# Performance work log

Measured on AMD Instinct MI355X. Metric: run time of the kernel, lower is better.

The kernel has to match this reference:

```python
import jax, jax.numpy as jnp
import numpy as np


def setup_inputs() -> dict:
    key = jax.random.key(0)
    ks = jax.random.split(key, 16)
    B, S, D, H = 32, 2048, 512, 512
    s = 1.0 / np.sqrt(H)
    inp = {
        "x": jax.random.normal(ks[0], (B, H), jnp.float32),
        "context": jax.random.normal(ks[1], (B, S, D), jnp.float32),
        "mask": jnp.zeros((B, S), jnp.bool_),  # False = valid position
        "Wi": jax.random.normal(ks[2], (H, H), jnp.float32) * s,
        "bi": jax.random.normal(ks[3], (H,), jnp.float32) * s,
        "Wc0": jax.random.normal(ks[4], (H, D), jnp.float32) * s,
        "bc0": jax.random.normal(ks[5], (H,), jnp.float32) * s,
        "Wc1": jax.random.normal(ks[6], (H, D), jnp.float32) * s,
        "bc1": jax.random.normal(ks[7], (H,), jnp.float32) * s,
        "Wc2": jax.random.normal(ks[8], (H, D), jnp.float32) * s,
        "bc2": jax.random.normal(ks[9], (H,), jnp.float32) * s,
        "Wc3": jax.random.normal(ks[10], (H, D), jnp.float32) * s,
        "bc3": jax.random.normal(ks[11], (H,), jnp.float32) * s,
        "V": jax.random.uniform(ks[12], (H,), jnp.float32, -s, s),
    }
    return inp


def reference(x, context, mask, Wi, bi, Wc0, bc0, Wc1, bc1, Wc2, bc2, Wc3, bc3, V):
    # mask: True = masked out in the original API; module flips it first.
    valid = ~mask  # [B, S], True = keep

    inp = (x @ Wi.T + bi)[:, :, None]  # [B, H, 1]

    def proj(W, b):
        # Conv1d(D, H, kernel=1) on context.permute(0,2,1) == token-wise GEMM
        return jnp.einsum("bsd,hd->bhs", context, W) + b[None, :, None]  # [B, H, S]

    ctx = jnp.concatenate(
        [proj(Wc0, bc0), proj(Wc1, bc1), proj(Wc2, bc2), proj(Wc3, bc3)], axis=2
    )  # [B, H, 4S]

    t = jnp.tanh(inp + ctx)                      # [B, H, 4S]
    att = jnp.einsum("h,bhs->bs", V, t)          # bmm(V[B,1,H], t).squeeze(1)
    att = 10.0 * jnp.tanh(att)                   # [B, 4S]

    valid4 = jnp.tile(valid, (1, 4))             # mask.repeat(1, 4)
    att = jnp.where(valid4, att, -jnp.inf)
    # torch.no_grad() around the masked fill detaches the rest of the graph
    att = jax.lax.stop_gradient(att)

    ans = jax.nn.softmax(att, axis=1)            # [B, 4S]
    p = jnp.max(ans, axis=1)
    indices = jnp.argmax(ans, axis=1)
    return indices[:, None], p[:, None], mask
```

## Files before the change

kernel.cpp:

```cpp
#include <hip/hip_runtime.h>
#include <math.h>

typedef __bf16 bf16x8 __attribute__((ext_vector_type(8)));
typedef float f32x4 __attribute__((ext_vector_type(4)));
typedef short short8v __attribute__((ext_vector_type(8)));

#define MARGIN 0.01f
#define NCAND 32

#define WAITL  do { asm volatile("s_waitcnt lgkmcnt(0)" ::: "memory"); __builtin_amdgcn_sched_barrier(0); } while (0)
#define WAITV0 do { asm volatile("s_waitcnt vmcnt(0)" ::: "memory"); __builtin_amdgcn_sched_barrier(0); } while (0)
#define WAITV4 do { asm volatile("s_waitcnt vmcnt(4)" ::: "memory"); __builtin_amdgcn_sched_barrier(0); } while (0)
#define WAITV8 do { asm volatile("s_waitcnt vmcnt(8)" ::: "memory"); __builtin_amdgcn_sched_barrier(0); } while (0)
#define BARR   do { __builtin_amdgcn_s_barrier(); __builtin_amdgcn_sched_barrier(0); } while (0)

__device__ __forceinline__ unsigned short f2bf(float f) {
  unsigned u = __float_as_uint(f);
  u += 0x7fffu + ((u >> 16) & 1u);
  return (unsigned short)(u >> 16);
}
__device__ __forceinline__ float tanh_fast(float x) {
  float e = __builtin_amdgcn_exp2f(x * 2.885390081777927f);
  return 1.f - 2.f * __builtin_amdgcn_rcpf(e + 1.f);
}
__device__ __forceinline__ void gl_lds16(const void* g, void* l) {
  __builtin_amdgcn_global_load_lds(
      (const __attribute__((address_space(1))) unsigned int*)g,
      (__attribute__((address_space(3))) unsigned int*)l, 16, 0, 0);
}
__device__ __forceinline__ float dpp_row_reduce(float v) {
  int x;
  x = __builtin_amdgcn_update_dpp(0, __builtin_bit_cast(int, v), 0x118, 0xf, 0xf, true);
  v += __builtin_bit_cast(float, x);
  x = __builtin_amdgcn_update_dpp(0, __builtin_bit_cast(int, v), 0x114, 0xf, 0xf, true);
  v += __builtin_bit_cast(float, x);
  x = __builtin_amdgcn_update_dpp(0, __builtin_bit_cast(int, v), 0x112, 0xf, 0xf, true);
  v += __builtin_bit_cast(float, x);
  x = __builtin_amdgcn_update_dpp(0, __builtin_bit_cast(int, v), 0x111, 0xf, 0xf, true);
  v += __builtin_bit_cast(float, x);
  return v;
}

__global__ __launch_bounds__(256) void prep_inp_k(const float* __restrict__ x,
    const float* __restrict__ Wi, const float* __restrict__ bi, float* __restrict__ inp) {
  int gid = blockIdx.x * 256 + threadIdx.x;
  int b = gid >> 9, h = gid & 511;
  const float* xr = x + b * 512;
  const float* wr = Wi + h * 512;
  float acc = bi[h];
  #pragma unroll 4
  for (int k = 0; k < 512; k += 4) {
    float4 xv = *(const float4*)(xr + k);
    float4 wv = *(const float4*)(wr + k);
    acc += xv.x * wv.x + xv.y * wv.y + xv.z * wv.z + xv.w * wv.w;
  }
  inp[gid] = acc;
}

__global__ __launch_bounds__(256) void prep_w_pack_k(const float* __restrict__ w0,
    const float* __restrict__ w1, const float* __restrict__ w2, const float* __restrict__ w3,
    short* __restrict__ Whi) {
  int gid = blockIdx.x * 256 + threadIdx.x;
  if (gid >= 131072) return;
  int c = gid & 3, row = (gid >> 2) & 255, TK = gid >> 10;
  int TN = TK >> 4, KS = TK & 15;
  int n = TN * 256 + row;
  int g = n >> 9, h = n & 511;
  const float* w = (g == 0) ? w0 : (g == 1) ? w1 : (g == 2) ? w2 : w3;
  const float* src = w + (size_t)h * 512 + KS * 32 + c * 8;
  float f[8];
  *(float4*)&f[0] = *(const float4*)(src);
  *(float4*)&f[4] = *(const float4*)(src + 4);
  short8v hv;
  #pragma unroll
  for (int i = 0; i < 8; ++i) hv[i] = (short)f2bf(f[i]);
  *(short8v*)(Whi + (size_t)gid * 8) = hv;
}

__global__ __launch_bounds__(256) void prep_ctx_pack_k(const float* __restrict__ ctx,
    short* __restrict__ Chi) {
  int gid = blockIdx.x * 256 + threadIdx.x;
  int c = gid & 3, row = (gid >> 2) & 255, TK = gid >> 10;
  int TM = TK >> 4, KS = TK & 15;
  size_t m = (size_t)TM * 256 + row;
  int k = KS * 32 + c * 8;
  float f[8];
  *(float4*)&f[0] = *(const float4*)(ctx + m * 512 + k);
  *(float4*)&f[4] = *(const float4*)(ctx + m * 512 + k + 4);
  short8v hv;
  #pragma unroll
  for (int i = 0; i < 8; ++i) hv[i] = (short)f2bf(f[i]);
  *(short8v*)(Chi + (size_t)gid * 8) = hv;
}

template<bool PRESPLIT>
__global__ __launch_bounds__(512, 2) void gemm_att_k(
    const float* __restrict__ ctx, const short* __restrict__ Chi,
    const short* __restrict__ Whi,
    const float* __restrict__ inp,
    const float* __restrict__ bc0, const float* __restrict__ bc1,
    const float* __restrict__ bc2, const float* __restrict__ bc3,
    const float* __restrict__ V, float* __restrict__ att) {
  __shared__ __align__(16) short smem[4][2][8192];
  __shared__ float sV[256], sPre[256];

  const int t = threadIdx.x;
  int d = blockIdx.x + (blockIdx.y << 3);
  int work = (d & 7) * 256 + (d >> 3);
  int mt = work >> 3, nt = work & 7;
  int b = mt >> 3;
  int g = nt >> 1, h0 = (nt & 1) * 256;

  if (t < 256) {
    const float* bc = (g == 0) ? bc0 : (g == 1) ? bc1 : (g == 2) ? bc2 : bc3;
    sV[t] = V[h0 + t];
    sPre[t] = inp[b * 512 + h0 + t] + bc[h0 + t];
  }

  const int toff = t * 8;
  auto stageA = [&](int tile) {
    const short* gA = Chi + (((size_t)mt * 16 + tile) << 13) + toff;
    short* lA = &smem[tile & 3][0][0];
    gl_lds16(gA,        lA + toff);
    gl_lds16(gA + 4096, lA + toff + 4096);
  };
  auto stageB = [&](int tile) {
    const short* gB = Whi + (((size_t)nt * 16 + tile) << 13) + toff;
    short* lB = &smem[tile & 3][1][0];
    gl_lds16(gB,        lB + toff);
    gl_lds16(gB + 4096, lB + toff + 4096);
  };
  auto stageA_reg = [&](int tile) {
    #pragma unroll
    for (int pass = 0; pass < 2; ++pass) {
      int cc = pass * 512 + t;
      int c = cc & 3, r = cc >> 2;
      int k = tile * 32 + c * 8;
      const float* src = ctx + ((size_t)mt * 256 + r) * 512 + k;
      float f[8];
      *(float4*)&f[0] = *(const float4*)src;
      *(float4*)&f[4] = *(const float4*)(src + 4);
      short8v hv;
      #pragma unroll
      for (int i = 0; i < 8; ++i) hv[i] = (short)f2bf(f[i]);
      *(short8v*)(&smem[tile & 3][0][r * 32 + c * 8]) = hv;
    }
  };

  f32x4 acc[8][4];
  #pragma unroll
  for (int i = 0; i < 8; ++i)
    #pragma unroll
    for (int j = 0; j < 4; ++j) acc[i][j] = (f32x4){0.f, 0.f, 0.f, 0.f};

  const int lane = t & 63, wid = t >> 6;
  const int wr = wid >> 2, wc = wid & 3;
  const int fr = lane & 15, fq = lane >> 4;
  const int abase = (wr * 128 + fr) * 32 + fq * 8;
  const int bbase = (wc * 64 + fr) * 32 + fq * 8;

  if constexpr (PRESPLIT) {
    stageA(0); stageB(0); stageA(1); stageB(1); stageA(2); stageB(2);
    WAITV8;
  } else {
    stageA_reg(0); stageB(0);
    WAITV0; WAITL;
  }
  BARR;

  #pragma unroll 4
  for (int tt = 0; tt < 16; ++tt) {
    const short* sa = &smem[tt & 3][0][0];
    const short* sb = &smem[tt & 3][1][0];
    bf16x8 a[8], b0, b1, b2, b3;
    #pragma unroll
    for (int mi = 0; mi < 8; ++mi)
      a[mi] = *(const bf16x8*)(sa + abase + mi * 512);
    b0 = *(const bf16x8*)(sb + bbase);
    b1 = *(const bf16x8*)(sb + bbase + 512);
    b2 = *(const bf16x8*)(sb + bbase + 1024);
    b3 = *(const bf16x8*)(sb + bbase + 1536);
    WAITL;
    __builtin_amdgcn_s_setprio(1);
    #pragma unroll
    for (int mi = 0; mi < 8; ++mi) {
      acc[mi][0] = __builtin_amdgcn_mfma_f32_16x16x32_bf16(a[mi], b0, acc[mi][0], 0, 0, 0);
      acc[mi][1] = __builtin_amdgcn_mfma_f32_16x16x32_bf16(a[mi], b1, acc[mi][1], 0, 0, 0);
    }
    #pragma unroll
    for (int mi = 0; mi < 8; ++mi) {
      acc[mi][2] = __builtin_amdgcn_mfma_f32_16x16x32_bf16(a[mi], b2, acc[mi][2], 0, 0, 0);
      acc[mi][3] = __builtin_amdgcn_mfma_f32_16x16x32_bf16(a[mi], b3, acc[mi][3], 0, 0, 0);
    }
    __builtin_amdgcn_s_setprio(0);
    __builtin_amdgcn_sched_barrier(0);
    if constexpr (PRESPLIT) {
      if (tt <= 12) { stageA(tt + 3); stageB(tt + 3); }
      if (tt <= 12)      { WAITV8; }
      else if (tt == 13) { WAITV4; }
      else if (tt == 14) { WAITV0; }
    } else {
      if (tt < 15) { stageA_reg(tt + 1); stageB(tt + 1); WAITV0; WAITL; }
    }
    BARR;
  }

  float vV[4], vP[4];
  #pragma unroll
  for (int ni = 0; ni < 4; ++ni) {
    int j = wc * 64 + ni * 16 + fr;
    vV[ni] = sV[j];
    vP[ni] = sPre[j];
  }
  size_t abatt = (size_t)b * 8192 + (size_t)g * 2048;
  #pragma unroll
  for (int mi = 0; mi < 8; ++mi) {
    #pragma unroll
    for (int r = 0; r < 4; ++r) {
      float sum = 0.f;
      #pragma unroll
      for (int ni = 0; ni < 4; ++ni)
        sum += vV[ni] * tanh_fast(vP[ni] + acc[mi][ni][r]);
      sum = dpp_row_reduce(sum);
      if (fr == 15) {
        int s = (mt * 256 + wr * 128 + mi * 16 + fq * 4 + r) & 2047;
        atomicAdd(&att[abatt + s], sum);
      }
    }
  }
}

__global__ __launch_bounds__(256) void tail_k(const float* __restrict__ att,
    const unsigned char* __restrict__ mask, const float* __restrict__ ctx,
    const float* __restrict__ Wc0, const float* __restrict__ Wc1,
    const float* __restrict__ Wc2, const float* __restrict__ Wc3,
    const float* __restrict__ bc0, const float* __restrict__ bc1,
    const float* __restrict__ bc2, const float* __restrict__ bc3,
    const float* __restrict__ inp, const float* __restrict__ V,
    float* __restrict__ out) {
  int b = blockIdx.x, t = threadIdx.x;
  __shared__ float sred[256];
  __shared__ float sctx[512];
  __shared__ int scnt;
  __shared__ int scand_j[NCAND];
  __shared__ float scand_a[NCAND];
  __shared__ float sexact[NCAND];

  if (t == 0) scnt = 0;
  float bm = -1e30f;
  for (int j = t; j < 8192; j += 256) {
    if (mask[b * 2048 + (j & 2047)]) continue;
    bm = fmaxf(bm, att[(size_t)b * 8192 + j]);
  }
  sred[t] = bm;
  __syncthreads();
  for (int s2 = 128; s2 > 0; s2 >>= 1) {
    if (t < s2) sred[t] = fmaxf(sred[t], sred[t + s2]);
    __syncthreads();
  }
  float mx = sred[0];
  float Lref = 10.f * tanhf(mx);
  __syncthreads();
  float se = 0.f;
  for (int j = t; j < 8192; j += 256) {
    if (mask[b * 2048 + (j & 2047)]) continue;
    float a = att[(size_t)b * 8192 + j];
    se += expf(10.f * tanhf(a) - Lref);
    if (a >= mx - MARGIN) {
      int slot = atomicAdd(&scnt, 1);
      if (slot < NCAND) { scand_j[slot] = j; scand_a[slot] = a; }
    }
  }
  sred[t] = se;
  __syncthreads();
  for (int s2 = 128; s2 > 0; s2 >>= 1) {
    if (t < s2) sred[t] += sred[t + s2];
    __syncthreads();
  }
  float den = sred[0];
  int n = min(scnt, NCAND);
  for (int j = t; j < 2048; j += 256)
    out[64 + b * 2048 + j] = mask[b * 2048 + j] ? 1.0f : 0.0f;
  for (int i = 0; i < n; ++i) {
    int jj = scand_j[i];
    int g = jj >> 11, s = jj & 2047;
    const float* W  = (g == 0) ? Wc0 : (g == 1) ? Wc1 : (g == 2) ? Wc2 : Wc3;
    const float* bc = (g == 0) ? bc0 : (g == 1) ? bc1 : (g == 2) ? bc2 : bc3;
    const float* cr = ctx + ((size_t)b * 2048 + s) * 512;
    __syncthreads();
    sctx[t] = cr[t];
    sctx[t + 256] = cr[t + 256];
    __syncthreads();
    float total = 0.f;
    #pragma unroll
    for (int hh = 0; hh < 2; ++hh) {
      int h = t + hh * 256;
      const float* wrp = W + (size_t)h * 512;
      float acc = 0.f;
      #pragma unroll 4
      for (int k = 0; k < 512; k += 4) {
        float4 wv = *(const float4*)(wrp + k);
        acc += wv.x * sctx[k] + wv.y * sctx[k + 1] + wv.z * sctx[k + 2] + wv.w * sctx[k + 3];
      }
      total += V[h] * tanhf(inp[b * 512 + h] + bc[h] + acc);
    }
    sred[t] = total;
    __syncthreads();
    for (int s2 = 128; s2 > 0; s2 >>= 1) {
      if (t < s2) sred[t] += sred[t + s2];
      __syncthreads();
    }
    if (t == 0) sexact[i] = sred[0];
  }
  __syncthreads();
  if (t == 0) {
    float dd = den, best = -1e30f;
    int bj = 0x7fffffff;
    for (int i = 0; i < n; ++i) {
      float e = sexact[i];
      int j = scand_j[i];
      dd += expf(10.f * tanhf(e) - Lref) - expf(10.f * tanhf(scand_a[i]) - Lref);
      if (e > best || (e == best && j < bj)) { best = e; bj = j; }
    }
    out[b] = (float)bj;
    out[32 + b] = expf(10.f * tanhf(best) - Lref) / dd;
  }
}

extern "C" void kernel_launch(void* const* d_in, const int* in_sizes, int n_in,
                              void* d_out, int out_size, void* d_ws, size_t ws_size,
                              hipStream_t stream) {
  const float* x    = (const float*)d_in[0];
  const float* ctx  = (const float*)d_in[1];
  const unsigned char* mask = (const unsigned char*)d_in[2];
  const float* Wi   = (const float*)d_in[3];
  const float* bi   = (const float*)d_in[4];
  const float* Wc0  = (const float*)d_in[5];
  const float* bc0  = (const float*)d_in[6];
  const float* Wc1  = (const float*)d_in[7];
  const float* bc1  = (const float*)d_in[8];
  const float* Wc2  = (const float*)d_in[9];
  const float* bc2  = (const float*)d_in[10];
  const float* Wc3  = (const float*)d_in[11];
  const float* bc3  = (const float*)d_in[12];
  const float* V    = (const float*)d_in[13];
  float* out = (float*)d_out;

  float* inp    = (float*)d_ws;
  float* att    = inp + 16384;
  short* Whi    = (short*)(att + 262144);
  short* Chi    = Whi + 1048576;
  size_t need = (size_t)((char*)(Chi + 33554432) - (char*)d_ws);
  bool presplit = ws_size >= need;

  hipMemsetAsync(att, 0, 262144 * sizeof(float), stream);
  prep_inp_k<<<64, 256, 0, stream>>>(x, Wi, bi, inp);
  prep_w_pack_k<<<512, 256, 0, stream>>>(Wc0, Wc1, Wc2, Wc3, Whi);
  if (presplit) {
    prep_ctx_pack_k<<<16384, 256, 0, stream>>>(ctx, Chi);
    gemm_att_k<true><<<dim3(8, 256), 512, 0, stream>>>(ctx, Chi, Whi,
        inp, bc0, bc1, bc2, bc3, V, att);
  } else {
    gemm_att_k<false><<<dim3(8, 256), 512, 0, stream>>>(ctx, nullptr, Whi,
        inp, bc0, bc1, bc2, bc3, V, att);
  }
  tail_k<<<32, 256, 0, stream>>>(att, mask, ctx, Wc0, Wc1, Wc2, Wc3,
      bc0, bc1, bc2, bc3, inp, V, out);
}
```

Baseline: 314.6 us.

## Load GEMM fragments directly from global into registers, dropping LDS staging

The presplit GEMM path no longer stages packed bf16 tiles through shared memory with a 4-deep async ring. Each wave now loads its MFMA fragments straight from the pre-packed global arrays into registers, double-buffered across K tiles with vmcnt-based waits. This removes LDS traffic and block barriers from the main loop. In exchange, data that several waves share is fetched redundantly from global/L2, and register pressure rises from holding two fragment sets. The fallback path is reduced to 2-stage LDS buffering.

After: 377.7 us. +20.0%, slower.

```diff
diff --git a/kernel.cpp b/kernel.cpp
--- a/kernel.cpp
+++ b/kernel.cpp
@@ -8,11 +8,10 @@
 #define MARGIN 0.01f
 #define NCAND 32
 
-#define WAITL  do { asm volatile("s_waitcnt lgkmcnt(0)" ::: "memory"); __builtin_amdgcn_sched_barrier(0); } while (0)
-#define WAITV0 do { asm volatile("s_waitcnt vmcnt(0)" ::: "memory"); __builtin_amdgcn_sched_barrier(0); } while (0)
-#define WAITV4 do { asm volatile("s_waitcnt vmcnt(4)" ::: "memory"); __builtin_amdgcn_sched_barrier(0); } while (0)
-#define WAITV8 do { asm volatile("s_waitcnt vmcnt(8)" ::: "memory"); __builtin_amdgcn_sched_barrier(0); } while (0)
-#define BARR   do { __builtin_amdgcn_s_barrier(); __builtin_amdgcn_sched_barrier(0); } while (0)
+#define WAITL   do { asm volatile("s_waitcnt lgkmcnt(0)" ::: "memory"); __builtin_amdgcn_sched_barrier(0); } while (0)
+#define WAITV0  do { asm volatile("s_waitcnt vmcnt(0)" ::: "memory"); __builtin_amdgcn_sched_barrier(0); } while (0)
+#define WAITV12 do { asm volatile("s_waitcnt vmcnt(12)" ::: "memory"); __builtin_amdgcn_sched_barrier(0); } while (0)
+#define BARR    do { __builtin_amdgcn_s_barrier(); __builtin_amdgcn_sched_barrier(0); } while (0)
 
 __device__ __forceinline__ unsigned short f2bf(float f) {
   unsigned u = __float_as_uint(f);
@@ -93,15 +92,34 @@
   *(short8v*)(Chi + (size_t)gid * 8) = hv;
 }
 
-template<bool PRESPLIT>
-__global__ __launch_bounds__(512, 2) void gemm_att_k(
-    const float* __restrict__ ctx, const short* __restrict__ Chi,
-    const short* __restrict__ Whi,
+#define LOADF(A_, B_, TT) do { \
+    const short* pa = Chi + aRegBase + (size_t)(TT) * 8192 + aoff; \
+    const short* pb = Whi + bRegBase + (size_t)(TT) * 8192 + boff; \
+    _Pragma("unroll") \
+    for (int mi = 0; mi < 8; ++mi) A_[mi] = *(const bf16x8*)(pa + mi * 512); \
+    _Pragma("unroll") \
+    for (int ni = 0; ni < 4; ++ni) B_[ni] = *(const bf16x8*)(pb + ni * 512); \
+  } while (0)
+
+#define MFMA_SET(A_, B_) do { \
+    __builtin_amdgcn_s_setprio(1); \
+    _Pragma("unroll") \
+    for (int mi = 0; mi < 8; ++mi) { \
+      acc[mi][0] = __builtin_amdgcn_mfma_f32_16x16x32_bf16(A_[mi], B_[0], acc[mi][0], 0, 0, 0); \
+      acc[mi][1] = __builtin_amdgcn_mfma_f32_16x16x32_bf16(A_[mi], B_[1], acc[mi][1], 0, 0, 0); \
+      acc[mi][2] = __builtin_amdgcn_mfma_f32_16x16x32_bf16(A_[mi], B_[2], acc[mi][2], 0, 0, 0); \
+      acc[mi][3] = __builtin_amdgcn_mfma_f32_16x16x32_bf16(A_[mi], B_[3], acc[mi][3], 0, 0, 0); \
+    } \
+    __builtin_amdgcn_s_setprio(0); \
+    __builtin_amdgcn_sched_barrier(0); \
+  } while (0)
+
+__global__ __launch_bounds__(512, 2) void gemm_direct_k(
+    const short* __restrict__ Chi, const short* __restrict__ Whi,
     const float* __restrict__ inp,
     const float* __restrict__ bc0, const float* __restrict__ bc1,
     const float* __restrict__ bc2, const float* __restrict__ bc3,
     const float* __restrict__ V, float* __restrict__ att) {
-  __shared__ __align__(16) short smem[4][2][8192];
   __shared__ float sV[256], sPre[256];
 
   const int t = threadIdx.x;
@@ -116,20 +134,83 @@
     sV[t] = V[h0 + t];
     sPre[t] = inp[b * 512 + h0 + t] + bc[h0 + t];
   }
-
+  __syncthreads();
+
+  const int lane = t & 63, wid = t >> 6;
+  const int wr = wid >> 2, wc = wid & 3;
+  const int fr = lane & 15, fq = lane >> 4;
+  const size_t aRegBase = (size_t)(mt * 16) * 8192;
+  const size_t bRegBase = (size_t)(nt * 16) * 8192;
+  const int aoff = (wr * 128 + fr) * 32 + fq * 8;
+  const int boff = (wc * 64 + fr) * 32 + fq * 8;
+
+  f32x4 acc[8][4];
+  #pragma unroll
+  for (int i = 0; i < 8; ++i)
+    #pragma unroll
+    for (int j = 0; j < 4; ++j) acc[i][j] = (f32x4){0.f, 0.f, 0.f, 0.f};
+
+  bf16x8 a0[8], b0v[4], a1[8], b1v[4];
+  LOADF(a0, b0v, 0);
+  #pragma unroll
+  for (int it = 0; it < 8; ++it) {
+    LOADF(a1, b1v, 2 * it + 1);
+    WAITV12;
+    MFMA_SET(a0, b0v);
+    if (it < 7) {
+      LOADF(a0, b0v, 2 * it + 2);
+      WAITV12;
+    } else {
+      WAITV0;
+    }
+    MFMA_SET(a1, b1v);
+  }
+
+  float vV[4], vP[4];
+  #pragma unroll
+  for (int ni = 0; ni < 4; ++ni) {
+    int j = wc * 64 + ni * 16 + fr;
+    vV[ni] = sV[j];
+    vP[ni] = sPre[j];
+  }
+  size_t abatt = (size_t)b * 8192 + (size_t)g * 2048;
+  #pragma unroll
+  for (int mi = 0; mi < 8; ++mi) {
+    #pragma unroll
+    for (int r = 0; r < 4; ++r) {
+      float sum = 0.f;
+      #pragma unroll
+      for (int ni = 0; ni < 4; ++ni)
+        sum += vV[ni] * tanh_fast(vP[ni] + acc[mi][ni][r]);
+      sum = dpp_row_reduce(sum);
+      if (fr == 15) {
+        int s = (mt * 256 + wr * 128 + mi * 16 + fq * 4 + r) & 2047;
+        atomicAdd(&att[abatt + s], sum);
+      }
+    }
+  }
+}
+
+__global__ __launch_bounds__(512, 2) void gemm_fallback_k(
+    const float* __restrict__ ctx, const short* __restrict__ Whi,
+    const float* __restrict__ inp,
+    const float* __restrict__ bc0, const float* __restrict__ bc1,
+    const float* __restrict__ bc2, const float* __restrict__ bc3,
+    const float* __restrict__ V, float* __restrict__ att) {
+  __shared__ __align__(16) short smem[2][2][8192];
+  __shared__ float sV[256], sPre[256];
+  const int t = threadIdx.x;
+  int d = blockIdx.x + (blockIdx.y << 3);
+  int work = (d & 7) * 256 + (d >> 3);
+  int mt = work >> 3, nt = work & 7;
+  int b = mt >> 3;
+  int g = nt >> 1, h0 = (nt & 1) * 256;
+  if (t < 256) {
+    const float* bc = (g == 0) ? bc0 : (g == 1) ? bc1 : (g == 2) ? bc2 : bc3;
+    sV[t] = V[h0 + t];
+    sPre[t] = inp[b * 512 + h0 + t] + bc[h0 + t];
+  }
   const int toff = t * 8;
-  auto stageA = [&](int tile) {
-    const short* gA = Chi + (((size_t)mt * 16 + tile) << 13) + toff;
-    short* lA = &smem[tile & 3][0][0];
-    gl_lds16(gA,        lA + toff);
-    gl_lds16(gA + 4096, lA + toff + 4096);
-  };
-  auto stageB = [&](int tile) {
-    const short* gB = Whi + (((size_t)nt * 16 + tile) << 13) + toff;
-    short* lB = &smem[tile & 3][1][0];
-    gl_lds16(gB,        lB + toff);
-    gl_lds16(gB + 4096, lB + toff + 4096);
-  };
   auto stageA_reg = [&](int tile) {
     #pragma unroll
     for (int pass = 0; pass < 2; ++pass) {
@@ -143,68 +224,44 @@
       short8v hv;
       #pragma unroll
       for (int i = 0; i < 8; ++i) hv[i] = (short)f2bf(f[i]);
-      *(short8v*)(&smem[tile & 3][0][r * 32 + c * 8]) = hv;
+      *(short8v*)(&smem[tile & 1][0][r * 32 + c * 8]) = hv;
     }
   };
-
+  auto stageB = [&](int tile) {
+    const short* gB = Whi + (((size_t)nt * 16 + tile) << 13) + toff;
+    short* lB = &smem[tile & 1][1][0];
+    gl_lds16(gB,        lB + toff);
+    gl_lds16(gB + 4096, lB + toff + 4096);
+  };
   f32x4 acc[8][4];
   #pragma unroll
   for (int i = 0; i < 8; ++i)
     #pragma unroll
     for (int j = 0; j < 4; ++j) acc[i][j] = (f32x4){0.f, 0.f, 0.f, 0.f};
-
   const int lane = t & 63, wid = t >> 6;
   const int wr = wid >> 2, wc = wid & 3;
   const int fr = lane & 15, fq = lane >> 4;
   const int abase = (wr * 128 + fr) * 32 + fq * 8;
   const int bbase = (wc * 64 + fr) * 32 + fq * 8;
-
-  if constexpr (PRESPLIT) {
-    stageA(0); stageB(0); stageA(1); stageB(1); stageA(2); stageB(2);
-    WAITV8;
-  } else {
-    stageA_reg(0); stageB(0);
-    WAITV0; WAITL;
-  }
+  stageA_reg(0); stageB(0);
+  WAITV0; WAITL;
   BARR;
-
-  #pragma unroll 4
   for (int tt = 0; tt < 16; ++tt) {
-    const short* sa = &smem[tt & 3][0][0];
-    const short* sb = &smem[tt & 3][1][0];
-    bf16x8 a[8], b0, b1, b2, b3;
+    const short* sa = &smem[tt & 1][0][0];
+    const short* sb = &smem[tt & 1][1][0];
+    bf16x8 a[8], bfr[4];
     #pragma unroll
     for (int mi = 0; mi < 8; ++mi)
       a[mi] = *(const bf16x8*)(sa + abase + mi * 512);
-    b0 = *(const bf16x8*)(sb + bbase);
-    b1 = *(const bf16x8*)(sb + bbase + 512);
-    b2 = *(const bf16x8*)(sb + bbase + 1024);
-    b3 = *(const bf16x8*)(sb + bbase + 1536);
+    bfr[0] = *(const bf16x8*)(sb + bbase);
+    bfr[1] = *(const bf16x8*)(sb + bbase + 512);
+    bfr[2] = *(const bf16x8*)(sb + bbase + 1024);
+    bfr[3] = *(const bf16x8*)(sb + bbase + 1536);
     WAITL;
-    __builtin_amdgcn_s_setprio(1);
-    #pragma unroll
-    for (int mi = 0; mi < 8; ++mi) {
-      acc[mi][0] = __builtin_amdgcn_mfma_f32_16x16x32_bf16(a[mi], b0, acc[mi][0], 0, 0, 0);
-      acc[mi][1] = __builtin_amdgcn_mfma_f32_16x16x32_bf16(a[mi], b1, acc[mi][1], 0, 0, 0);
-    }
-    #pragma unroll
-    for (int mi = 0; mi < 8; ++mi) {
-      acc[mi][2] = __builtin_amdgcn_mfma_f32_16x16x32_bf16(a[mi], b2, acc[mi][2], 0, 0, 0);
-      acc[mi][3] = __builtin_amdgcn_mfma_f32_16x16x32_bf16(a[mi], b3, acc[mi][3], 0, 0, 0);
-    }
-    __builtin_amdgcn_s_setprio(0);
-    __builtin_amdgcn_sched_barrier(0);
-    if constexpr (PRESPLIT) {
-      if (tt <= 12) { stageA(tt + 3); stageB(tt + 3); }
-      if (tt <= 12)      { WAITV8; }
-      else if (tt == 13) { WAITV4; }
-      else if (tt == 14) { WAITV0; }
-    } else {
-      if (tt < 15) { stageA_reg(tt + 1); stageB(tt + 1); WAITV0; WAITL; }
-    }
+    MFMA_SET(a, bfr);
+    if (tt < 15) { stageA_reg(tt + 1); stageB(tt + 1); WAITV0; WAITL; }
     BARR;
   }
-
   float vV[4], vP[4];
   #pragma unroll
   for (int ni = 0; ni < 4; ++ni) {
@@ -358,10 +415,10 @@
   prep_w_pack_k<<<512, 256, 0, stream>>>(Wc0, Wc1, Wc2, Wc3, Whi);
   if (presplit) {
     prep_ctx_pack_k<<<16384, 256, 0, stream>>>(ctx, Chi);
-    gemm_att_k<true><<<dim3(8, 256), 512, 0, stream>>>(ctx, Chi, Whi,
+    gemm_direct_k<<<dim3(8, 256), 512, 0, stream>>>(Chi, Whi,
         inp, bc0, bc1, bc2, bc3, V, att);
   } else {
-    gemm_att_k<false><<<dim3(8, 256), 512, 0, stream>>>(ctx, nullptr, Whi,
+    gemm_fallback_k<<<dim3(8, 256), 512, 0, stream>>>(ctx, Whi,
         inp, bc0, bc1, bc2, bc3, V, att);
   }
   tail_k<<<32, 256, 0, stream>>>(att, mask, ctx, Wc0, Wc1, Wc2, Wc3,
```

## Drop context pre-pack pass, convert context inside GEMM, merge prep kernels

Applied to the files above, without the earlier changes.

Removes the separate pass that converted the full context tensor to packed bf16 in workspace. The GEMM now always loads fp32 context through registers and converts it per tile, giving up the 3-deep async LDS pipeline for single-tile staging. The two small prep kernels are merged into one launch, and the tail kernel is widened to 1024 threads. The aim is to avoid writing and re-reading a large bf16 copy of context, at the cost of less load/compute overlap in the GEMM.

Result: slower. 339.5 us (+7.9%).

```diff
diff --git a/kernel.cpp b/kernel.cpp
--- a/kernel.cpp
+++ b/kernel.cpp
@@ -10,8 +10,6 @@
 
 #define WAITL  do { asm volatile("s_waitcnt lgkmcnt(0)" ::: "memory"); __builtin_amdgcn_sched_barrier(0); } while (0)
 #define WAITV0 do { asm volatile("s_waitcnt vmcnt(0)" ::: "memory"); __builtin_amdgcn_sched_barrier(0); } while (0)
-#define WAITV4 do { asm volatile("s_waitcnt vmcnt(4)" ::: "memory"); __builtin_amdgcn_sched_barrier(0); } while (0)
-#define WAITV8 do { asm volatile("s_waitcnt vmcnt(8)" ::: "memory"); __builtin_amdgcn_sched_barrier(0); } while (0)
 #define BARR   do { __builtin_amdgcn_s_barrier(); __builtin_amdgcn_sched_barrier(0); } while (0)
 
 __device__ __forceinline__ unsigned short f2bf(float f) {
@@ -41,62 +39,46 @@
   return v;
 }
 
-__global__ __launch_bounds__(256) void prep_inp_k(const float* __restrict__ x,
-    const float* __restrict__ Wi, const float* __restrict__ bi, float* __restrict__ inp) {
-  int gid = blockIdx.x * 256 + threadIdx.x;
-  int b = gid >> 9, h = gid & 511;
-  const float* xr = x + b * 512;
-  const float* wr = Wi + h * 512;
-  float acc = bi[h];
-  #pragma unroll 4
-  for (int k = 0; k < 512; k += 4) {
-    float4 xv = *(const float4*)(xr + k);
-    float4 wv = *(const float4*)(wr + k);
-    acc += xv.x * wv.x + xv.y * wv.y + xv.z * wv.z + xv.w * wv.w;
-  }
-  inp[gid] = acc;
-}
-
-__global__ __launch_bounds__(256) void prep_w_pack_k(const float* __restrict__ w0,
-    const float* __restrict__ w1, const float* __restrict__ w2, const float* __restrict__ w3,
-    short* __restrict__ Whi) {
-  int gid = blockIdx.x * 256 + threadIdx.x;
-  if (gid >= 131072) return;
-  int c = gid & 3, row = (gid >> 2) & 255, TK = gid >> 10;
-  int TN = TK >> 4, KS = TK & 15;
-  int n = TN * 256 + row;
-  int g = n >> 9, h = n & 511;
-  const float* w = (g == 0) ? w0 : (g == 1) ? w1 : (g == 2) ? w2 : w3;
-  const float* src = w + (size_t)h * 512 + KS * 32 + c * 8;
-  float f[8];
-  *(float4*)&f[0] = *(const float4*)(src);
-  *(float4*)&f[4] = *(const float4*)(src + 4);
-  short8v hv;
-  #pragma unroll
-  for (int i = 0; i < 8; ++i) hv[i] = (short)f2bf(f[i]);
-  *(short8v*)(Whi + (size_t)gid * 8) = hv;
-}
-
-__global__ __launch_bounds__(256) void prep_ctx_pack_k(const float* __restrict__ ctx,
-    short* __restrict__ Chi) {
-  int gid = blockIdx.x * 256 + threadIdx.x;
-  int c = gid & 3, row = (gid >> 2) & 255, TK = gid >> 10;
-  int TM = TK >> 4, KS = TK & 15;
-  size_t m = (size_t)TM * 256 + row;
-  int k = KS * 32 + c * 8;
-  float f[8];
-  *(float4*)&f[0] = *(const float4*)(ctx + m * 512 + k);
-  *(float4*)&f[4] = *(const float4*)(ctx + m * 512 + k + 4);
-  short8v hv;
-  #pragma unroll
-  for (int i = 0; i < 8; ++i) hv[i] = (short)f2bf(f[i]);
-  *(short8v*)(Chi + (size_t)gid * 8) = hv;
-}
-
-template<bool PRESPLIT>
-__global__ __launch_bounds__(512, 2) void gemm_att_k(
-    const float* __restrict__ ctx, const short* __restrict__ Chi,
-    const short* __restrict__ Whi,
+__global__ __launch_bounds__(256) void prep_small_k(
+    const float* __restrict__ x, const float* __restrict__ Wi,
+    const float* __restrict__ bi,
+    const float* __restrict__ w0, const float* __restrict__ w1,
+    const float* __restrict__ w2, const float* __restrict__ w3,
+    short* __restrict__ Whi, float* __restrict__ inp) {
+  int bid = blockIdx.x;
+  if (bid < 512) {
+    int gid = bid * 256 + threadIdx.x;
+    int c = gid & 3, row = (gid >> 2) & 255, TK = gid >> 10;
+    int TN = TK >> 4, KS = TK & 15;
+    int n = TN * 256 + row;
+    int g = n >> 9, h = n & 511;
+    const float* w = (g == 0) ? w0 : (g == 1) ? w1 : (g == 2) ? w2 : w3;
+    const float* src = w + (size_t)h * 512 + KS * 32 + c * 8;
+    float f[8];
+    *(float4*)&f[0] = *(const float4*)(src);
+    *(float4*)&f[4] = *(const float4*)(src + 4);
+    short8v hv;
+    #pragma unroll
+    for (int i = 0; i < 8; ++i) hv[i] = (short)f2bf(f[i]);
+    *(short8v*)(Whi + (size_t)gid * 8) = hv;
+  } else {
+    int gid = (bid - 512) * 256 + threadIdx.x;
+    int b = gid >> 9, h = gid & 511;
+    const float* xr = x + b * 512;
+    const float* wr = Wi + h * 512;
+    float acc = bi[h];
+    #pragma unroll 4
+    for (int k = 0; k < 512; k += 4) {
+      float4 xv = *(const float4*)(xr + k);
+      float4 wv = *(const float4*)(wr + k);
+      acc += xv.x * wv.x + xv.y * wv.y + xv.z * wv.z + xv.w * wv.w;
+    }
+    inp[gid] = acc;
+  }
+}
+
+__global__ __launch_bounds__(512, 2) void gemm_fused_k(
+    const float* __restrict__ ctx, const short* __restrict__ Whi,
     const float* __restrict__ inp,
     const float* __restrict__ bc0, const float* __restrict__ bc1,
     const float* __restrict__ bc2, const float* __restrict__ bc3,
@@ -119,18 +101,6 @@
 
   const int toff = t * 8;
   auto stageA = [&](int tile) {
-    const short* gA = Chi + (((size_t)mt * 16 + tile) << 13) + toff;
-    short* lA = &smem[tile & 3][0][0];
-    gl_lds16(gA,        lA + toff);
-    gl_lds16(gA + 4096, lA + toff + 4096);
-  };
-  auto stageB = [&](int tile) {
-    const short* gB = Whi + (((size_t)nt * 16 + tile) << 13) + toff;
-    short* lB = &smem[tile & 3][1][0];
-    gl_lds16(gB,        lB + toff);
-    gl_lds16(gB + 4096, lB + toff + 4096);
-  };
-  auto stageA_reg = [&](int tile) {
     #pragma unroll
     for (int pass = 0; pass < 2; ++pass) {
       int cc = pass * 512 + t;
@@ -146,6 +116,12 @@
       *(short8v*)(&smem[tile & 3][0][r * 32 + c * 8]) = hv;
     }
   };
+  auto stageB = [&](int tile) {
+    const short* gB = Whi + (((size_t)nt * 16 + tile) << 13) + toff;
+    short* lB = &smem[tile & 3][1][0];
+    gl_lds16(gB,        lB + toff);
+    gl_lds16(gB + 4096, lB + toff + 4096);
+  };
 
   f32x4 acc[8][4];
   #pragma unroll
@@ -159,13 +135,8 @@
   const int abase = (wr * 128 + fr) * 32 + fq * 8;
   const int bbase = (wc * 64 + fr) * 32 + fq * 8;
 
-  if constexpr (PRESPLIT) {
-    stageA(0); stageB(0); stageA(1); stageB(1); stageA(2); stageB(2);
-    WAITV8;
-  } else {
-    stageA_reg(0); stageB(0);
-    WAITV0; WAITL;
-  }
+  stageA(0); stageB(0);
+  WAITV0; WAITL;
   BARR;
 
   #pragma unroll 4
@@ -194,13 +165,10 @@
     }
     __builtin_amdgcn_s_setprio(0);
     __builtin_amdgcn_sched_barrier(0);
-    if constexpr (PRESPLIT) {
-      if (tt <= 12) { stageA(tt + 3); stageB(tt + 3); }
-      if (tt <= 12)      { WAITV8; }
-      else if (tt == 13) { WAITV4; }
-      else if (tt == 14) { WAITV0; }
-    } else {
-      if (tt < 15) { stageA_reg(tt + 1); stageB(tt + 1); WAITV0; WAITL; }
+    if (tt < 15) {
+      stageA(tt + 1);
+      stageB(tt + 1);
+      WAITV0; WAITL;
     }
     BARR;
   }
@@ -230,7 +198,7 @@
   }
 }
 
-__global__ __launch_bounds__(256) void tail_k(const float* __restrict__ att,
+__global__ __launch_bounds__(1024) void tail_k(const float* __restrict__ att,
     const unsigned char* __restrict__ mask, const float* __restrict__ ctx,
     const float* __restrict__ Wc0, const float* __restrict__ Wc1,
     const float* __restrict__ Wc2, const float* __restrict__ Wc3,
@@ -239,7 +207,7 @@
     const float* __restrict__ inp, const float* __restrict__ V,
     float* __restrict__ out) {
   int b = blockIdx.x, t = threadIdx.x;
-  __shared__ float sred[256];
+  __shared__ float sred[1024];
   __shared__ float sctx[512];
   __shared__ int scnt;
   __shared__ int scand_j[NCAND];
@@ -248,13 +216,13 @@
 
   if (t == 0) scnt = 0;
   float bm = -1e30f;
-  for (int j = t; j < 8192; j += 256) {
+  for (int j = t; j < 8192; j += 1024) {
     if (mask[b * 2048 + (j & 2047)]) continue;
     bm = fmaxf(bm, att[(size_t)b * 8192 + j]);
   }
   sred[t] = bm;
   __syncthreads();
-  for (int s2 = 128; s2 > 0; s2 >>= 1) {
+  for (int s2 = 512; s2 > 0; s2 >>= 1) {
     if (t < s2) sred[t] = fmaxf(sred[t], sred[t + s2]);
     __syncthreads();
   }
@@ -262,7 +230,7 @@
   float Lref = 10.f * tanhf(mx);
   __syncthreads();
   float se = 0.f;
-  for (int j = t; j < 8192; j += 256) {
+  for (int j = t; j < 8192; j += 1024) {
     if (mask[b * 2048 + (j & 2047)]) continue;
     float a = att[(size_t)b * 8192 + j];
     se += expf(10.f * tanhf(a) - Lref);
@@ -273,13 +241,13 @@
   }
   sred[t] = se;
   __syncthreads();
-  for (int s2 = 128; s2 > 0; s2 >>= 1) {
+  for (int s2 = 512; s2 > 0; s2 >>= 1) {
     if (t < s2) sred[t] += sred[t + s2];
     __syncthreads();
   }
   float den = sred[0];
   int n = min(scnt, NCAND);
-  for (int j = t; j < 2048; j += 256)
+  for (int j = t; j < 2048; j += 1024)
     out[64 + b * 2048 + j] = mask[b * 2048 + j] ? 1.0f : 0.0f;
   for (int i = 0; i < n; ++i) {
     int jj = scand_j[i];
@@ -288,25 +256,22 @@
     const float* bc = (g == 0) ? bc0 : (g == 1) ? bc1 : (g == 2) ? bc2 : bc3;
     const float* cr = ctx + ((size_t)b * 2048 + s) * 512;
     __syncthreads();
-    sctx[t] = cr[t];
-    sctx[t + 256] = cr[t + 256];
+    if (t < 512) sctx[t] = cr[t];
     __syncthreads();
     float total = 0.f;
-    #pragma unroll
-    for (int hh = 0; hh < 2; ++hh) {
-      int h = t + hh * 256;
-      const float* wrp = W + (size_t)h * 512;
+    if (t < 512) {
+      const float* wrp = W + (size_t)t * 512;
       float acc = 0.f;
       #pragma unroll 4
       for (int k = 0; k < 512; k += 4) {
         float4 wv = *(const float4*)(wrp + k);
         acc += wv.x * sctx[k] + wv.y * sctx[k + 1] + wv.z * sctx[k + 2] + wv.w * sctx[k + 3];
       }
-      total += V[h] * tanhf(inp[b * 512 + h] + bc[h] + acc);
+      total = V[t] * tanhf(inp[b * 512 + t] + bc[t] + acc);
     }
     sred[t] = total;
     __syncthreads();
-    for (int s2 = 128; s2 > 0; s2 >>= 1) {
+    for (int s2 = 512; s2 > 0; s2 >>= 1) {
       if (t < s2) sred[t] += sred[t + s2];
       __syncthreads();
     }
@@ -346,24 +311,14 @@
   const float* V    = (const float*)d_in[13];
   float* out = (float*)d_out;
 
-  float* inp    = (float*)d_ws;
-  float* att    = inp + 16384;
-  short* Whi    = (short*)(att + 262144);
-  short* Chi    = Whi + 1048576;
-  size_t need = (size_t)((char*)(Chi + 33554432) - (char*)d_ws);
-  bool presplit = ws_size >= need;
+  float* inp = (float*)d_ws;
+  float* att = inp + 16384;
+  short* Whi = (short*)(att + 262144);
 
   hipMemsetAsync(att, 0, 262144 * sizeof(float), stream);
-  prep_inp_k<<<64, 256, 0, stream>>>(x, Wi, bi, inp);
-  prep_w_pack_k<<<512, 256, 0, stream>>>(Wc0, Wc1, Wc2, Wc3, Whi);
-  if (presplit) {
-    prep_ctx_pack_k<<<16384, 256, 0, stream>>>(ctx, Chi);
-    gemm_att_k<true><<<dim3(8, 256), 512, 0, stream>>>(ctx, Chi, Whi,
-        inp, bc0, bc1, bc2, bc3, V, att);
-  } else {
-    gemm_att_k<false><<<dim3(8, 256), 512, 0, stream>>>(ctx, nullptr, Whi,
-        inp, bc0, bc1, bc2, bc3, V, att);
-  }
-  tail_k<<<32, 256, 0, stream>>>(att, mask, ctx, Wc0, Wc1, Wc2, Wc3,
+  prep_small_k<<<576, 256, 0, stream>>>(x, Wi, bi, Wc0, Wc1, Wc2, Wc3, Whi, inp);
+  gemm_fused_k<<<dim3(8, 256), 512, 0, stream>>>(ctx, Whi,
+      inp, bc0, bc1, bc2, bc3, V, att);
+  tail_k<<<32, 1024, 0, stream>>>(att, mask, ctx, Wc0, Wc1, Wc2, Wc3,
       bc0, bc1, bc2, bc3, inp, V, out);
 }
```
